# Kernel optimization log

Measured on AMD Instinct MI355X. Metric: run time of the kernel, lower is better.

## Reference

```python
import jax, jax.numpy as jnp
import numpy as np

N, E, B = 10000, 20000, 500
H, NODE_D, EDGE_D, L = 64, 11, 5, 3
BN_EPS = 1e-5
STEPS = 3  # Set2Set processing steps


def setup_inputs() -> dict:
    key = jax.random.key(0)
    ks = jax.random.split(key, 16)
    s = lambda k, shape, fan: (jax.random.normal(k, shape, jnp.float32) / np.sqrt(fan)).astype(jnp.float32)
    p = {}
    p["x"] = jax.random.normal(ks[0], (N, NODE_D), jnp.float32)
    p["edge_index"] = jax.random.randint(ks[1], (2, E), 0, N)
    p["edge_attr"] = jax.random.uniform(ks[2], (E, EDGE_D), dtype=jnp.float32)
    p["batch"] = jnp.sort(jax.random.randint(ks[3], (N,), 0, B))
    # node encoder
    p["W_enc"] = s(ks[4], (NODE_D, H), NODE_D); p["b_enc"] = jnp.zeros((H,), jnp.float32)
    # per-layer NNConv block params (stacked over L layers)
    p["eW1"] = s(ks[5], (L, EDGE_D, H), EDGE_D); p["eb1"] = jnp.zeros((L, H), jnp.float32)
    p["eW2"] = s(ks[6], (L, H, H * H), H);       p["eb2"] = jnp.zeros((L, H * H), jnp.float32)
    p["root"] = s(ks[7], (L, H, H), H);          p["cbias"] = jnp.zeros((L, H), jnp.float32)
    p["gamma"] = jnp.ones((L, H), jnp.float32);  p["beta"] = jnp.zeros((L, H), jnp.float32)
    # Set2Set LSTM (input 2H, hidden H)
    p["Wih"] = s(ks[8], (4 * H, 2 * H), 2 * H); p["Whh"] = s(ks[9], (4 * H, H), H)
    p["bih"] = jnp.zeros((4 * H,), jnp.float32); p["bhh"] = jnp.zeros((4 * H,), jnp.float32)
    p["hW1"] = s(ks[10], (2 * H, H), 2 * H);   p["hb1"] = jnp.zeros((H,), jnp.float32)
    p["hW2"] = s(ks[11], (H, H // 2), H);      p["hb2"] = jnp.zeros((H // 2,), jnp.float32)
    p["hW3"] = s(ks[12], (H // 2, 1), H // 2); p["hb3"] = jnp.zeros((1,), jnp.float32)
    return p


def _forward(x, edge_attr, W_enc, b_enc, eW1, eb1, eW2, eb2, root, cbias, gamma, beta,
             Wih, Whh, bih, bhh, hW1, hb1, hW2, hb2, hW3, hb3, edge_index, batch):
    src, dst = edge_index[0], edge_index[1]
    # in-degree for mean aggregation (0-degree nodes -> 0 output, clamp avoids /0)
    deg = jax.ops.segment_sum(jnp.ones((E,), jnp.float32), dst, num_segments=N)
    deg = jnp.maximum(deg, 1.0)[:, None]

    h = jax.nn.relu(x @ W_enc + b_enc)  # [N, H]

    for l in range(L):
        residual = h
        # edge MLP -> per-edge [H, H] weight matrix
        e1 = jax.nn.relu(edge_attr @ eW1[l] + eb1[l])          # [E, H]
        W = (e1 @ eW2[l] + eb2[l]).reshape(E, H, H)            # [E, H, H]
        msg = jnp.einsum('eh,eho->eo', h[src], W)              # per-edge matvec
        agg = jax.ops.segment_sum(msg, dst, num_segments=N) / deg
        h = agg + h @ root[l] + cbias[l]                       # NNConv (root + bias)
        # BatchNorm1d (training-mode batch stats, biased var), eval-mode dropout (no-op)
        mu = jnp.mean(h, axis=0)
        var = jnp.mean((h - mu) ** 2, axis=0)
        h = (h - mu) * jax.lax.rsqrt(var + BN_EPS) * gamma[l] + beta[l]
        h = jax.nn.relu(h) + residual

    # Set2Set readout
    q_star = jnp.zeros((B, 2 * H), jnp.float32)
    hl = jnp.zeros((B, H), jnp.float32)
    cl = jnp.zeros((B, H), jnp.float32)
    for _ in range(STEPS):
        gates = q_star @ Wih.T + bih + hl @ Whh.T + bhh
        i, f, g, o = jnp.split(gates, 4, axis=1)
        cl = jax.nn.sigmoid(f) * cl + jax.nn.sigmoid(i) * jnp.tanh(g)
        hl = jax.nn.sigmoid(o) * jnp.tanh(cl)
        q = hl                                                  # [B, H]
        e = jnp.sum(h * q[batch], axis=-1)                      # [N]
        m = jax.ops.segment_max(e, batch, num_segments=B)
        ex = jnp.exp(e - m[batch])
        sden = jax.ops.segment_sum(ex, batch, num_segments=B)
        a = ex / sden[batch]                                    # per-graph softmax
        r = jax.ops.segment_sum(a[:, None] * h, batch, num_segments=B)
        q_star = jnp.concatenate([q, r], axis=1)

    # head
    z = jax.nn.relu(q_star @ hW1 + hb1)
    z = jax.nn.relu(z @ hW2 + hb2)
    out = z @ hW3 + hb3
    return out.reshape(-1)  # [B]


def reference(x, edge_index, edge_attr, batch, W_enc, b_enc, eW1, eb1, eW2, eb2, root,
              cbias, gamma, beta, Wih, Whh, bih, bhh, hW1, hb1, hW2, hb2, hW3, hb3):
    return _forward(x, edge_attr, W_enc, b_enc, eW1, eb1, eW2, eb2, root, cbias, gamma,
                    beta, Wih, Whh, bih, bhh, hW1, hb1, hW2, hb2, hW3, hb3,
                    edge_index, batch)
```

## Files before the change

### kernel.cpp

```cpp
#include <hip/hip_runtime.h>
#include <math.h>

#define ND 11
#define ED 5
#define NL 3
#define NSTEPS 3
#define BN_EPS 1e-5f
#define NSLAB 32

typedef _Float16 half8 __attribute__((ext_vector_type(8)));
typedef float f32x4 __attribute__((ext_vector_type(4)));

__device__ __forceinline__ float sigm(float x) { return 1.0f / (1.0f + expf(-x)); }

__global__ __launch_bounds__(256) void k_setup(
    const float* __restrict__ x, const float* __restrict__ Wenc,
    const float* __restrict__ benc, float* __restrict__ h0,
    _Float16* __restrict__ hh, int N,
    const int* __restrict__ dst, float* __restrict__ deg, int E,
    const int* __restrict__ batch, int* __restrict__ ptr, int B,
    const float* __restrict__ Wih, const float* __restrict__ Whh,
    const float* __restrict__ bih, const float* __restrict__ bhh,
    float* __restrict__ WihT, float* __restrict__ WhhT, float* __restrict__ gbias,
    const float* __restrict__ w2, const float* __restrict__ b2,
    _Float16* __restrict__ w2P, float* __restrict__ zp, long NZ,
    int nbEnc, int nbDeg, int nbPtr, int nbPackW, int nbPack3) {
  int bid = blockIdx.x;
  const int tid = threadIdx.x;
  if (bid < nbEnc) {
    int idx = bid * 256 + tid;
    if (idx < N * 64) {
      int n = idx >> 6, j = idx & 63;
      float acc = benc[j];
#pragma unroll
      for (int i = 0; i < ND; ++i) acc = fmaf(x[n * ND + i], Wenc[i * 64 + j], acc);
      float v = fmaxf(acc, 0.0f);
      h0[idx] = v;
      hh[idx] = (_Float16)v;
    }
    return;
  }
  bid -= nbEnc;
  if (bid < nbDeg) {
    int e = bid * 256 + tid;
    if (e < E) atomicAdd(&deg[dst[e]], 1.0f);
    return;
  }
  bid -= nbDeg;
  if (bid < nbPtr) {
    int n = bid * 256 + tid;
    if (n < N) {
      int b = batch[n];
      int pb = (n == 0) ? -1 : batch[n - 1];
      for (int g = pb + 1; g <= b; ++g) ptr[g] = n;
      if (n == N - 1)
        for (int g = b + 1; g <= B; ++g) ptr[g] = N;
    }
    return;
  }
  bid -= nbPtr;
  if (bid < nbPackW) {
    int idx = bid * 256 + tid;
    if (idx < 128 * 256) {
      int i = idx >> 8, g = idx & 255;
      WihT[i * 256 + g] = Wih[g * 128 + i];
    } else if (idx < 192 * 256) {
      int j = idx - 128 * 256;
      int i = j >> 8, g = j & 255;
      WhhT[i * 256 + g] = Whh[g * 64 + i];
    } else if (idx < 192 * 256 + 256) {
      int g = idx - 192 * 256;
      gbias[g] = bih[g] + bhh[g];
    }
    return;
  }
  bid -= nbPackW;
  if (bid < nbPack3) {
    int lay = bid / 130;
    int idx = (bid % 130) * 256 + tid;
    int l = idx & 63;
    int f = (idx >> 6) & 7;
    int s = idx >> 9;
    int nf = f >> 1, kf = f & 1;
    const float* srow = (s < 64) ? (w2 + (size_t)lay * 64 * 4096 + (size_t)s * 4096)
                                 : (b2 + (size_t)lay * 4096);
    int o = nf * 16 + (l & 15);
    int hb = kf * 32 + (l >> 4) * 8;
    half8 v;
#pragma unroll
    for (int j = 0; j < 8; ++j) v[j] = (_Float16)srow[(hb + j) * 64 + o];
    *(half8*)(w2P + ((size_t)lay * 65 * 8 * 64 + idx) * 8) = v;
    return;
  }
  bid -= nbPack3;
  {
    long i4 = ((long)bid * 256 + tid) * 4;
    if (i4 + 3 < NZ) *(float4*)(zp + i4) = make_float4(0.f, 0.f, 0.f, 0.f);
    else for (; i4 < NZ; ++i4) zp[i4] = 0.f;
  }
}

__global__ void k_zdeg(float* __restrict__ deg, int N) {
  int i = blockIdx.x * blockDim.x + threadIdx.x;
  if (i < N) deg[i] = 0.f;
}

__global__ __launch_bounds__(256) void k_scan(const float* __restrict__ deg,
                                              int* __restrict__ dptr,
                                              int* __restrict__ cursor, int N) {
  __shared__ int wsum[4];
  __shared__ int s_carry;
  const int tid = threadIdx.x, lane = tid & 63, w = tid >> 6;
  if (tid == 0) s_carry = 0;
  __syncthreads();
  for (int base = 0; base < N; base += 1024) {
    int n0 = base + tid * 4;
    int v[4];
    int s = 0;
#pragma unroll
    for (int i = 0; i < 4; ++i) { v[i] = (n0 + i < N) ? (int)deg[n0 + i] : 0; s += v[i]; }
    int sc = s;
#pragma unroll
    for (int off = 1; off < 64; off <<= 1) {
      int t = __shfl_up(sc, off);
      if (lane >= off) sc += t;
    }
    if (lane == 63) wsum[w] = sc;
    __syncthreads();
    int wpre = 0;
    for (int ww = 0; ww < w; ++ww) wpre += wsum[ww];
    int excl = s_carry + wpre + sc - s;
#pragma unroll
    for (int i = 0; i < 4; ++i) {
      if (n0 + i < N) { dptr[n0 + i] = excl; cursor[n0 + i] = excl; }
      excl += v[i];
    }
    __syncthreads();
    if (tid == 255) s_carry += wsum[0] + wsum[1] + wsum[2] + wsum[3];
    __syncthreads();
  }
  if (threadIdx.x == 0) dptr[N] = s_carry;
}

__global__ void k_fill(const int* __restrict__ dst, const int* __restrict__ src,
                       int* __restrict__ cursor, int* __restrict__ perm,
                       int* __restrict__ srcP, int* __restrict__ dstP, int E) {
  int e = blockIdx.x * blockDim.x + threadIdx.x;
  if (e < E) {
    int d = dst[e];
    int slot = atomicAdd(&cursor[d], 1);
    perm[slot] = e;
    srcP[slot] = src[e];
    dstP[slot] = d;
  }
}

__global__ __launch_bounds__(256) void k_hmat(
    const float* __restrict__ hn, const float* __restrict__ hp,
    const float* __restrict__ slab, const float* __restrict__ gm,
    const float* __restrict__ bt, float* __restrict__ hout,
    _Float16* __restrict__ hh, int N) {
  __shared__ float stats[128];
  const int tid = threadIdx.x;
  if (tid < 128) {
    float s = 0.f;
#pragma unroll
    for (int sl = 0; sl < NSLAB; ++sl) s += slab[sl * 128 + tid];
    stats[tid] = s;
  }
  __syncthreads();
  int idx = blockIdx.x * 256 + tid;
  if (idx >= N * 64) return;
  int o = idx & 63;
  float invN = 1.0f / (float)N;
  float mu = stats[o] * invN;
  float var = stats[64 + o] * invN - mu * mu;
  float rs = rsqrtf(var + BN_EPS) * gm[o];
  float v = fmaxf((hn[idx] - mu) * rs + bt[o], 0.f) + hp[idx];
  hout[idx] = v;
  hh[idx] = (_Float16)v;
}

__global__ __launch_bounds__(512, 2) void k_msgagg(
    const float* __restrict__ ea, const int* __restrict__ perm,
    const float* __restrict__ eW1l, const float* __restrict__ eb1l,
    const _Float16* __restrict__ hh, const int* __restrict__ srcP,
    const int* __restrict__ dstP, const int* __restrict__ dptr,
    const _Float16* __restrict__ w2P, float* __restrict__ agg, int E, int N) {
  __shared__ _Float16 e1t[65][64];
  __shared__ float tileH[2][64][66];
  __shared__ float eat[64][ED];
  __shared__ float w1s[ED * 64];
  __shared__ float b1s[64];

  const int tid = threadIdx.x;
  const int wid = tid >> 6, l = tid & 63;
  const int half = wid >> 2, quad = wid & 3;
  const int lo = l & 15, lg = l >> 4;
  const int e0 = blockIdx.x * 64;

  half8 hsf[4][2];
#pragma unroll
  for (int m = 0; m < 4; ++m) {
    int s = e0 + m * 16 + lo;
    if (s < E) {
      const _Float16* hr = hh + (size_t)srcP[s] * 64;
      hsf[m][0] = *(const half8*)(hr + lg * 8);
      hsf[m][1] = *(const half8*)(hr + 32 + lg * 8);
    } else {
      half8 z = {0, 0, 0, 0, 0, 0, 0, 0};
      hsf[m][0] = z;
      hsf[m][1] = z;
    }
  }

  if (tid < ED * 64) w1s[tid] = eW1l[tid];
  else if (tid < ED * 64 + 64) b1s[tid - ED * 64] = eb1l[tid - ED * 64];
  if (tid >= 448) {
    int s = e0 + (tid - 448);
    if (s < E) {
      int e = perm[s];
#pragma unroll
      for (int i = 0; i < ED; ++i) eat[tid - 448][i] = ea[(size_t)e * ED + i];
    } else {
#pragma unroll
      for (int i = 0; i < ED; ++i) eat[tid - 448][i] = 0.f;
    }
  }
  __syncthreads();

  for (int idx = tid; idx < 65 * 64; idx += 512) {
    int el = idx & 63, k = idx >> 6;
    float v = 1.0f;
    if (k < 64) {
      v = b1s[k];
#pragma unroll
      for (int i = 0; i < ED; ++i) v = fmaf(eat[el][i], w1s[i * 64 + k], v);
      v = fmaxf(v, 0.f);
    }
    e1t[k][el] = (_Float16)v;
  }
  __syncthreads();

  const int kb = half ? 32 : 0;
  f32x4 acc[4] = {};
  const half8* wp = (const half8*)w2P;
  half8 Br[4][2];
  _Float16 sr[4][4];
#pragma unroll
  for (int d = 0; d < 4; ++d) {
    const int k = kb + d;
    Br[d][0] = wp[((size_t)k * 8 + quad * 2 + 0) * 64 + l];
    Br[d][1] = wp[((size_t)k * 8 + quad * 2 + 1) * 64 + l];
#pragma unroll
    for (int m = 0; m < 4; ++m)
      sr[d][m] = (half && d == 0) ? (_Float16)0.f : e1t[k][m * 16 + lo];
  }
#pragma unroll 33
  for (int i = 0; i < 33; ++i) {
    const int d = i & 3;
#pragma unroll
    for (int m = 0; m < 4; ++m) {
      const _Float16 s16 = sr[d][m];
      half8 A0 = hsf[m][0] * s16;
      half8 A1 = hsf[m][1] * s16;
      acc[m] = __builtin_amdgcn_mfma_f32_16x16x32_f16(A0, Br[d][0], acc[m], 0, 0, 0);
      acc[m] = __builtin_amdgcn_mfma_f32_16x16x32_f16(A1, Br[d][1], acc[m], 0, 0, 0);
    }
    if (i + 4 < 33) {
      const int kn = kb + i + 4;
      Br[d][0] = wp[((size_t)kn * 8 + quad * 2 + 0) * 64 + l];
      Br[d][1] = wp[((size_t)kn * 8 + quad * 2 + 1) * 64 + l];
#pragma unroll
      for (int m = 0; m < 4; ++m) sr[d][m] = e1t[kn][m * 16 + lo];
    }
  }

#pragma unroll
  for (int m = 0; m < 4; ++m)
#pragma unroll
    for (int r = 0; r < 4; ++r)
      tileH[half][m * 16 + lg * 4 + r][quad * 16 + lo] = acc[m][r];
  __syncthreads();

  const int o = tid & 63, r8 = tid >> 6;
  const int lastSlot = (e0 + 63 < E) ? (e0 + 63) : (E - 1);
  int nLo = dstP[e0], nHi = dstP[lastSlot];
  nLo = (nLo < 0) ? 0 : ((nLo >= N) ? N - 1 : nLo);
  nHi = (nHi < 0) ? 0 : ((nHi >= N) ? N - 1 : nHi);
  for (int nn = nLo + r8; nn <= nHi; nn += 8) {
    int d0 = dptr[nn], d1 = dptr[nn + 1];
    d0 = (d0 < 0) ? 0 : d0;
    d1 = (d1 > E) ? E : d1;
    int j0 = (d0 > e0) ? d0 : e0;
    int j1 = (d1 < e0 + 64) ? d1 : (e0 + 64);
    float sum = 0.f;
    for (int j = j0; j < j1; ++j) sum += tileH[0][j - e0][o] + tileH[1][j - e0][o];
    float* dp = agg + (size_t)nn * 64 + o;
    if (d0 < e0 || d1 > e0 + 64) { if (j1 > j0) atomicAdd(dp, sum); }
    else *dp = sum;
  }
}

__global__ __launch_bounds__(256) void k_update(
    const float* __restrict__ hcur, float* __restrict__ agg,
    const float* __restrict__ deg, const float* __restrict__ root,
    const float* __restrict__ cb, float* __restrict__ hn_out,
    float* __restrict__ slab_out, int N) {
  __shared__ float hrow[16][64];
  __shared__ float red[2][256];
  const int tid = threadIdx.x, o = tid & 63, r = tid >> 6;
  const int nb = blockIdx.x * 16;
#pragma unroll
  for (int ii = 0; ii < 4; ++ii) {
    int n = nb + ii * 4 + r;
    hrow[ii * 4 + r][o] = (n < N) ? hcur[(size_t)n * 64 + o] : 0.f;
  }
  __syncthreads();
  float acc[4] = {0.f, 0.f, 0.f, 0.f};
  for (int c = 0; c < 64; ++c) {
    float rv = root[c * 64 + o];
#pragma unroll
    for (int ii = 0; ii < 4; ++ii) acc[ii] = fmaf(hrow[ii * 4 + r][c], rv, acc[ii]);
  }
  float s = 0.f, ss = 0.f;
  const float cbv = cb[o];
#pragma unroll
  for (int ii = 0; ii < 4; ++ii) {
    int n = nb + ii * 4 + r;
    if (n < N) {
      float a = agg[(size_t)n * 64 + o];
      agg[(size_t)n * 64 + o] = 0.f;
      float v = acc[ii] + cbv + a / fmaxf(deg[n], 1.0f);
      hn_out[(size_t)n * 64 + o] = v;
      s += v;
      ss += v * v;
    }
  }
  red[0][tid] = s;
  red[1][tid] = ss;
  __syncthreads();
  if (r == 0) {
    float t0 = red[0][o] + red[0][64 + o] + red[0][128 + o] + red[0][192 + o];
    float t1 = red[1][o] + red[1][64 + o] + red[1][128 + o] + red[1][192 + o];
    float* sl = slab_out + (size_t)(blockIdx.x & (NSLAB - 1)) * 128;
    atomicAdd(&sl[o], t0);
    atomicAdd(&sl[64 + o], t1);
  }
}

__global__ __launch_bounds__(256) void k_s2s_all(
    const float* __restrict__ hn2, const float* __restrict__ h2,
    const float* __restrict__ slab2, const float* __restrict__ gm,
    const float* __restrict__ bt, const int* __restrict__ ptr,
    const float* __restrict__ WihT, const float* __restrict__ WhhT,
    const float* __restrict__ gbias,
    const float* __restrict__ hW1, const float* __restrict__ hb1,
    const float* __restrict__ hW2, const float* __restrict__ hb2,
    const float* __restrict__ hW3, const float* __restrict__ hb3,
    float* __restrict__ out, int N) {
  __shared__ float stats[128];
  __shared__ float qs[128];
  __shared__ float hlc[64], clc[64];
  __shared__ float gates[256];
  __shared__ float qv[64];
  __shared__ float redM[4], redS[4];
  __shared__ float redR[4][64];
  __shared__ float z1[64], z2[32];
  const int b = blockIdx.x, tid = threadIdx.x;
  const int wid = tid >> 6, lane = tid & 63;

  if (tid < 128) {
    float s = 0.f;
#pragma unroll
    for (int sl = 0; sl < NSLAB; ++sl) s += slab2[sl * 128 + tid];
    stats[tid] = s;
    qs[tid] = 0.f;
  }
  if (tid < 64) { hlc[tid] = 0.f; clc[tid] = 0.f; }
  __syncthreads();
  const float invN = 1.0f / (float)N;
  const float muR = stats[lane] * invN;
  const float varR = stats[64 + lane] * invN - muR * muR;
  const float rsR = rsqrtf(varR + BN_EPS) * gm[lane];
  const float btR = bt[lane];
  const int beg = ptr[b], end = ptr[b + 1];

  for (int step = 0; step < NSTEPS; ++step) {
    float g = gbias[tid];
    for (int i = 0; i < 128; ++i) g = fmaf(qs[i], WihT[i * 256 + tid], g);
    for (int i = 0; i < 64; ++i) g = fmaf(hlc[i], WhhT[i * 256 + tid], g);
    gates[tid] = g;
    __syncthreads();
    if (tid < 64) {
      float ig = sigm(gates[tid]);
      float fg = sigm(gates[64 + tid]);
      float gg = tanhf(gates[128 + tid]);
      float og = sigm(gates[192 + tid]);
      float c = fg * clc[tid] + ig * gg;
      clc[tid] = c;
      float hnew = og * tanhf(c);
      hlc[tid] = hnew;
      qv[tid] = hnew;
    }
    __syncthreads();
    const float q = qv[lane];
    float mw = -INFINITY;
    for (int n = beg + wid; n < end; n += 4) {
      float hv = fmaxf((hn2[(size_t)n * 64 + lane] - muR) * rsR + btR, 0.f) +
                 h2[(size_t)n * 64 + lane];
      float p = hv * q;
#pragma unroll
      for (int s = 32; s; s >>= 1) p += __shfl_xor(p, s);
      mw = fmaxf(mw, p);
    }
    if (lane == 0) redM[wid] = mw;
    __syncthreads();
    const float m = fmaxf(fmaxf(redM[0], redM[1]), fmaxf(redM[2], redM[3]));
    float ssum = 0.f, racc = 0.f;
    for (int n = beg + wid; n < end; n += 4) {
      float hv = fmaxf((hn2[(size_t)n * 64 + lane] - muR) * rsR + btR, 0.f) +
                 h2[(size_t)n * 64 + lane];
      float p = hv * q;
#pragma unroll
      for (int s = 32; s; s >>= 1) p += __shfl_xor(p, s);
      float a = expf(p - m);
      ssum += a;
      racc = fmaf(a, hv, racc);
    }
    if (lane == 0) redS[wid] = ssum;
    redR[wid][lane] = racc;
    __syncthreads();
    if (tid < 128) {
      if (tid < 64) {
        qs[tid] = qv[tid];
      } else {
        int o2 = tid - 64;
        float rsum = redR[0][o2] + redR[1][o2] + redR[2][o2] + redR[3][o2];
        float sd = redS[0] + redS[1] + redS[2] + redS[3];
        qs[tid] = (end > beg) ? rsum / sd : 0.0f;
      }
    }
    __syncthreads();
  }

  if (tid < 64) {
    float a = hb1[tid];
    for (int i = 0; i < 128; ++i) a = fmaf(qs[i], hW1[i * 64 + tid], a);
    z1[tid] = fmaxf(a, 0.0f);
  }
  __syncthreads();
  if (tid < 32) {
    float a2 = hb2[tid];
    for (int i = 0; i < 64; ++i) a2 = fmaf(z1[i], hW2[i * 32 + tid], a2);
    z2[tid] = fmaxf(a2, 0.0f);
  }
  __syncthreads();
  if (tid < 64) {
    float p = (tid < 32) ? z2[tid] * hW3[tid] : 0.0f;
#pragma unroll
    for (int s = 32; s; s >>= 1) p += __shfl_xor(p, s);
    if (tid == 0) out[b] = p + hb3[0];
  }
}

extern "C" void kernel_launch(void* const* d_in, const int* in_sizes, int n_in,
                              void* d_out, int out_size, void* d_ws, size_t ws_size,
                              hipStream_t stream) {
  const float* x = (const float*)d_in[0];
  const int* eidx = (const int*)d_in[1];
  const float* ea = (const float*)d_in[2];
  const int* batch = (const int*)d_in[3];
  const float* Wenc = (const float*)d_in[4];
  const float* benc = (const float*)d_in[5];
  const float* eW1 = (const float*)d_in[6];
  const float* eb1 = (const float*)d_in[7];
  const float* eW2 = (const float*)d_in[8];
  const float* eb2 = (const float*)d_in[9];
  const float* root = (const float*)d_in[10];
  const float* cbias = (const float*)d_in[11];
  const float* gamma = (const float*)d_in[12];
  const float* beta = (const float*)d_in[13];
  const float* Wih = (const float*)d_in[14];
  const float* Whh = (const float*)d_in[15];
  const float* bih = (const float*)d_in[16];
  const float* bhh = (const float*)d_in[17];
  const float* hW1 = (const float*)d_in[18];
  const float* hb1 = (const float*)d_in[19];
  const float* hW2 = (const float*)d_in[20];
  const float* hb2 = (const float*)d_in[21];
  const float* hW3 = (const float*)d_in[22];
  const float* hb3 = (const float*)d_in[23];

  const int N = in_sizes[0] / ND;
  const int E = in_sizes[1] / 2;
  const int B = out_size;
  const int* srcp = eidx;
  const int* dstp = eidx + E;
  const int Etiles = (E + 63) / 64;

  float* ws = (float*)d_ws;
  float* deg = ws;
  float* agg = deg + N;
  float* bnslab = agg + (size_t)N * 64;
  const long NZ = (long)((size_t)N * 64 + NL * NSLAB * 128);
  float* h0 = bnslab + NL * NSLAB * 128;
  float* h1 = h0 + (size_t)N * 64;
  float* h2 = h1 + (size_t)N * 64;
  float* hn0 = h2 + (size_t)N * 64;
  float* hn1 = hn0 + (size_t)N * 64;
  float* hn2 = hn1 + (size_t)N * 64;
  _Float16* w2P = (_Float16*)(hn2 + (size_t)N * 64);
  _Float16* hhalf = w2P + (size_t)3 * 65 * 8 * 64 * 8;
  float* WihT = (float*)(hhalf + (size_t)N * 64);
  float* WhhT = WihT + 128 * 256;
  float* gbias = WhhT + 64 * 256;
  int* dptr = (int*)(gbias + 256);
  int* cursor = dptr + N + 1;
  int* perm = cursor + N;
  int* srcP = perm + E;
  int* dstP = srcP + E;
  int* ptr = dstP + E;

  const int nbEnc = (N * 64 + 255) / 256;
  const int nbDeg = (E + 255) / 256;
  const int nbPtr = (N + 255) / 256;
  const int nbPackW = (192 * 256 + 256 + 255) / 256;
  const int nbPack3 = 130 * NL;
  const int nbZero = (int)((NZ / 4 + 255) / 256);

  k_zdeg<<<(N + 255) / 256, 256, 0, stream>>>(deg, N);
  k_setup<<<nbEnc + nbDeg + nbPtr + nbPackW + nbPack3 + nbZero, 256, 0, stream>>>(
      x, Wenc, benc, h0, hhalf, N, dstp, deg, E, batch, ptr, B,
      Wih, Whh, bih, bhh, WihT, WhhT, gbias, eW2, eb2, w2P, agg, NZ,
      nbEnc, nbDeg, nbPtr, nbPackW, nbPack3);
  k_scan<<<1, 256, 0, stream>>>(deg, dptr, cursor, N);
  k_fill<<<(E + 255) / 256, 256, 0, stream>>>(dstp, srcp, cursor, perm, srcP, dstP, E);

  float* hbuf[3] = {h0, h1, h2};
  float* hnbuf[3] = {hn0, hn1, hn2};
  for (int l = 0; l < NL; ++l) {
    float* slab_l = bnslab + (size_t)l * NSLAB * 128;
    const _Float16* w2_l = w2P + (size_t)l * 65 * 8 * 64 * 8;
    if (l > 0) {
      k_hmat<<<(N * 64 + 255) / 256, 256, 0, stream>>>(
          hnbuf[l - 1], hbuf[l - 1], bnslab + (size_t)(l - 1) * NSLAB * 128,
          gamma + (l - 1) * 64, beta + (l - 1) * 64, hbuf[l], hhalf, N);
    }
    k_msgagg<<<Etiles, 512, 0, stream>>>(ea, perm, eW1 + (size_t)l * ED * 64,
                                         eb1 + (size_t)l * 64, hhalf, srcP, dstP, dptr,
                                         w2_l, agg, E, N);
    k_update<<<(N + 15) / 16, 256, 0, stream>>>(hbuf[l], agg, deg,
                                                root + (size_t)l * 64 * 64,
                                                cbias + l * 64, hnbuf[l], slab_l, N);
  }

  k_s2s_all<<<B, 256, 0, stream>>>(hn2, h2, bnslab + (size_t)2 * NSLAB * 128,
                                   gamma + 2 * 64, beta + 2 * 64, ptr, WihT, WhhT, gbias,
                                   hW1, hb1, hW2, hb2, hW3, hb3, (float*)d_out, N);
}
```

Measured before the change: 216.1 us.

## Stage normalized node features in LDS for Set2Set and restructure attention

The Set2Set kernel now computes the batch-norm/ReLU/residual node features once per graph into a padded shared-memory tile, for graphs of up to 256 nodes. Previously it re-read them from global memory twice per step. Attention scores are computed one node per thread, followed by block reductions for max and sum, and one thread per output channel does the readout. Graphs larger than the cap fall back to the old path. This trades a large LDS allocation, which can lower occupancy, and a serial per-channel readout loop for fewer global reads.

```diff
diff --git a/kernel.cpp b/kernel.cpp
--- a/kernel.cpp
+++ b/kernel.cpp
@@ -7,6 +7,7 @@
 #define NSTEPS 3
 #define BN_EPS 1e-5f
 #define NSLAB 32
+#define CAP 256
 
 typedef _Float16 half8 __attribute__((ext_vector_type(8)));
 typedef float f32x4 __attribute__((ext_vector_type(4)));
@@ -359,11 +360,15 @@
     const float* __restrict__ hW2, const float* __restrict__ hb2,
     const float* __restrict__ hW3, const float* __restrict__ hb3,
     float* __restrict__ out, int N) {
+  __shared__ float hvs[CAP * 65];
   __shared__ float stats[128];
+  __shared__ float mu_s[64], rs_s[64], bt_s[64];
   __shared__ float qs[128];
   __shared__ float hlc[64], clc[64];
   __shared__ float gates[256];
   __shared__ float qv[64];
+  __shared__ float ev[256];
+  __shared__ float av[CAP];
   __shared__ float redM[4], redS[4];
   __shared__ float redR[4][64];
   __shared__ float z1[64], z2[32];
@@ -379,12 +384,29 @@
   }
   if (tid < 64) { hlc[tid] = 0.f; clc[tid] = 0.f; }
   __syncthreads();
-  const float invN = 1.0f / (float)N;
-  const float muR = stats[lane] * invN;
-  const float varR = stats[64 + lane] * invN - muR * muR;
-  const float rsR = rsqrtf(varR + BN_EPS) * gm[lane];
-  const float btR = bt[lane];
-  const int beg = ptr[b], end = ptr[b + 1];
+  if (tid < 64) {
+    float invN = 1.0f / (float)N;
+    float mu = stats[tid] * invN;
+    float var = stats[64 + tid] * invN - mu * mu;
+    mu_s[tid] = mu;
+    rs_s[tid] = rsqrtf(var + BN_EPS) * gm[tid];
+    bt_s[tid] = bt[tid];
+  }
+  __syncthreads();
+  int beg = ptr[b], end = ptr[b + 1];
+  if (beg < 0) beg = 0;
+  if (end > N) end = N;
+  const int nn = (end > beg) ? (end - beg) : 0;
+  const bool big = nn > CAP;
+
+  if (!big) {
+    for (int idx = tid; idx < nn * 64; idx += 256) {
+      int n = idx >> 6, o = idx & 63;
+      size_t g = (size_t)(beg + n) * 64 + o;
+      hvs[n * 65 + o] = fmaxf((hn2[g] - mu_s[o]) * rs_s[o] + bt_s[o], 0.f) + h2[g];
+    }
+  }
+  __syncthreads();
 
   for (int step = 0; step < NSTEPS; ++step) {
     float g = gbias[tid];
@@ -404,44 +426,89 @@
       qv[tid] = hnew;
     }
     __syncthreads();
-    const float q = qv[lane];
-    float mw = -INFINITY;
-    for (int n = beg + wid; n < end; n += 4) {
-      float hv = fmaxf((hn2[(size_t)n * 64 + lane] - muR) * rsR + btR, 0.f) +
-                 h2[(size_t)n * 64 + lane];
-      float p = hv * q;
-#pragma unroll
-      for (int s = 32; s; s >>= 1) p += __shfl_xor(p, s);
-      mw = fmaxf(mw, p);
-    }
-    if (lane == 0) redM[wid] = mw;
-    __syncthreads();
-    const float m = fmaxf(fmaxf(redM[0], redM[1]), fmaxf(redM[2], redM[3]));
-    float ssum = 0.f, racc = 0.f;
-    for (int n = beg + wid; n < end; n += 4) {
-      float hv = fmaxf((hn2[(size_t)n * 64 + lane] - muR) * rsR + btR, 0.f) +
-                 h2[(size_t)n * 64 + lane];
-      float p = hv * q;
-#pragma unroll
-      for (int s = 32; s; s >>= 1) p += __shfl_xor(p, s);
-      float a = expf(p - m);
-      ssum += a;
-      racc = fmaf(a, hv, racc);
-    }
-    if (lane == 0) redS[wid] = ssum;
-    redR[wid][lane] = racc;
-    __syncthreads();
-    if (tid < 128) {
+
+    if (!big) {
+      if (tid < nn) {
+        float s = 0.f;
+#pragma unroll 8
+        for (int o = 0; o < 64; ++o) s = fmaf(hvs[tid * 65 + o], qv[o], s);
+        ev[tid] = s;
+      } else {
+        ev[tid] = -INFINITY;
+      }
+      __syncthreads();
       if (tid < 64) {
-        qs[tid] = qv[tid];
-      } else {
-        int o2 = tid - 64;
-        float rsum = redR[0][o2] + redR[1][o2] + redR[2][o2] + redR[3][o2];
-        float sd = redS[0] + redS[1] + redS[2] + redS[3];
-        qs[tid] = (end > beg) ? rsum / sd : 0.0f;
+        float m4 = fmaxf(fmaxf(ev[tid], ev[64 + tid]), fmaxf(ev[128 + tid], ev[192 + tid]));
+#pragma unroll
+        for (int s = 32; s; s >>= 1) m4 = fmaxf(m4, __shfl_xor(m4, s));
+        if (tid == 0) redM[0] = m4;
       }
-    }
-    __syncthreads();
+      __syncthreads();
+      const float m = redM[0];
+      float a = 0.f;
+      if (tid < nn) { a = expf(ev[tid] - m); av[tid] = a; }
+      __syncthreads();
+      ev[tid] = a;
+      __syncthreads();
+      if (tid < 64) {
+        float s4 = ev[tid] + ev[64 + tid] + ev[128 + tid] + ev[192 + tid];
+#pragma unroll
+        for (int s = 32; s; s >>= 1) s4 += __shfl_xor(s4, s);
+        if (tid == 0) redS[0] = s4;
+      }
+      __syncthreads();
+      const float sden = redS[0];
+      if (tid < 128) {
+        if (tid < 64) {
+          qs[tid] = qv[tid];
+        } else {
+          int o = tid - 64;
+          float r = 0.f;
+          for (int n = 0; n < nn; ++n) r = fmaf(av[n], hvs[n * 65 + o], r);
+          qs[tid] = (nn > 0) ? r / sden : 0.f;
+        }
+      }
+      __syncthreads();
+    } else {
+      const float q = qv[lane];
+      float mw = -INFINITY;
+      for (int n = beg + wid; n < end; n += 4) {
+        float hv = fmaxf((hn2[(size_t)n * 64 + lane] - mu_s[lane]) * rs_s[lane] + bt_s[lane],
+                         0.f) + h2[(size_t)n * 64 + lane];
+        float p = hv * q;
+#pragma unroll
+        for (int s = 32; s; s >>= 1) p += __shfl_xor(p, s);
+        mw = fmaxf(mw, p);
+      }
+      if (lane == 0) redM[wid] = mw;
+      __syncthreads();
+      const float m = fmaxf(fmaxf(redM[0], redM[1]), fmaxf(redM[2], redM[3]));
+      float ssum = 0.f, racc = 0.f;
+      for (int n = beg + wid; n < end; n += 4) {
+        float hv = fmaxf((hn2[(size_t)n * 64 + lane] - mu_s[lane]) * rs_s[lane] + bt_s[lane],
+                         0.f) + h2[(size_t)n * 64 + lane];
+        float p = hv * q;
+#pragma unroll
+        for (int s = 32; s; s >>= 1) p += __shfl_xor(p, s);
+        float a = expf(p - m);
+        ssum += a;
+        racc = fmaf(a, hv, racc);
+      }
+      if (lane == 0) redS[wid] = ssum;
+      redR[wid][lane] = racc;
+      __syncthreads();
+      if (tid < 128) {
+        if (tid < 64) {
+          qs[tid] = qv[tid];
+        } else {
+          int o2 = tid - 64;
+          float rsum = redR[0][o2] + redR[1][o2] + redR[2][o2] + redR[3][o2];
+          float sd = redS[0] + redS[1] + redS[2] + redS[3];
+          qs[tid] = (end > beg) ? rsum / sd : 0.0f;
+        }
+      }
+      __syncthreads();
+    }
   }
 
   if (tid < 64) {
```

Result: faster. 204.4 us (-5.4%).
